# Kernel tuning notes

Hardware: AMD Instinct MI355X
Metric: run time of the kernel (lower is better)

Reference implementation:

```python
import jax, jax.numpy as jnp
import numpy as np

N, D = 8192, 256

def _gram_rbf(x, y, sigma):
    x2 = jnp.sum(x * x, axis=-1)                      # [N]
    y2 = jnp.sum(y * y, axis=-1)                      # [M]
    xy = jnp.einsum('nd,md->nm', x, y)                # [N,M] GEMM
    sq = x2[:, None] + y2[None, :] - 2.0 * xy
    return jnp.exp(-sq / sigma)

def setup_inputs() -> dict:
    key = jax.random.key(0)
    k1, k2 = jax.random.split(key)
    return {
        'input': jax.random.normal(k1, (N, D), dtype=jnp.float32),
        'target': jax.random.normal(k2, (N, D), dtype=jnp.float32) + 0.5,
        'sigma': 256,
    }

def reference(input, target, sigma):
    XX = _gram_rbf(input, input, sigma)
    YY = _gram_rbf(target, target, sigma)
    XY = _gram_rbf(input, target, sigma)
    return jnp.mean(XX) + jnp.mean(YY) - 2.0 * jnp.mean(XY)
```

## Files before the change

### kernel.cpp

```cpp
#include <hip/hip_runtime.h>
#include <hip/hip_bf16.h>
#include <stdint.h>
#include <stddef.h>


#define N_PTS   8192
#define DIM     256
#define TWO_N   16384
#define CSTRIDE 16

#define AS1 __attribute__((address_space(1)))
#define AS3 __attribute__((address_space(3)))

typedef __attribute__((ext_vector_type(4))) float f32x4;

__global__ __launch_bounds__(256) void mmd_prep(const float* __restrict__ X,
                                                const float* __restrict__ Y,
                                                const int* __restrict__ sigmap,
                                                unsigned char* __restrict__ Zf8,
                                                float* __restrict__ n2,
                                                float* __restrict__ out) {
    if (blockIdx.x == 0 && threadIdx.x == 0) out[0] = 0.0f;

    const int wave = threadIdx.x >> 6;
    const int lane = threadIdx.x & 63;
    const int row  = blockIdx.x * 4 + wave;

    const float* src = (row < N_PTS) ? (X + (size_t)row * DIM)
                                     : (Y + (size_t)(row - N_PTS) * DIM);
    float4 v = ((const float4*)src)[lane];

    float s = v.x * v.x + v.y * v.y + v.z * v.z + v.w * v.w;
#pragma unroll
    for (int off = 32; off; off >>= 1) s += __shfl_down(s, off, 64);
    if (lane == 0) {
        const float c2 = -1.4426950408889634f / (float)(*sigmap);
        n2[row] = c2 * s;
    }

    const int p01 = __builtin_amdgcn_cvt_pk_fp8_f32(v.x, v.y, 0, false);
    const int p23 = __builtin_amdgcn_cvt_pk_fp8_f32(v.z, v.w, 0, false);
    const unsigned int pk = ((unsigned)p01 & 0xffffu) | ((unsigned)p23 << 16);
    *(unsigned int*)(Zf8 + (size_t)row * DIM + (size_t)lane * 4) = pk;
}

__global__ __launch_bounds__(256, 2) void mmd_main(const unsigned char* __restrict__ Zf8,
                                                   const float* __restrict__ n2,
                                                   const int* __restrict__ sigmap,
                                                   float* __restrict__ out) {
    __shared__ char smem_b[65536];
    __shared__ float wsum[4];

    const int bid = (int)blockIdx.x;
    const int br  = 127 - (bid >> 4);
    const int cc  = bid & 15;
    if (cc > br) return;

    const int t    = threadIdx.x;
    const int wave = t >> 6;
    const int lane = t & 63;
    const int wm   = wave >> 1;
    const int wn   = wave & 1;
    const int g    = lane >> 4;
    const int ml   = lane & 15;
    const int rowBase = br * 128;

    const float m2 = 2.8853900817779268f / (float)(*sigmap);

    {
        const int colBase0 = cc * 128;
#pragma unroll
        for (int i = 0; i < 8; ++i) {
            const int cidx = i * 256 + t;
            const int col  = cidx >> 4;
            const int s    = cidx & 15;
            const int gc   = s ^ (col & 15);
            const unsigned char* gp = Zf8 + (size_t)(colBase0 + col) * DIM + gc * 16;
            __builtin_amdgcn_global_load_lds((const AS1 void*)gp,
                                             (AS3 void*)(smem_b + (size_t)cidx * 16), 16, 0, 0);
        }
    }

    long af[4][8];
#pragma unroll
    for (int mt = 0; mt < 4; ++mt) {
        const unsigned char* rp =
            Zf8 + (size_t)(rowBase + wm * 64 + mt * 16 + ml) * DIM + g * 8;
#pragma unroll
        for (int kc = 0; kc < 8; ++kc)
            af[mt][kc] = *(const long*)(rp + kc * 32);
    }
    float a_i[4][4];
#pragma unroll
    for (int mt = 0; mt < 4; ++mt)
#pragma unroll
        for (int rr = 0; rr < 4; ++rr)
            a_i[mt][rr] = n2[rowBase + wm * 64 + mt * 16 + g * 4 + rr];

    float block_acc = 0.0f;
    const int brX = (br < 64);
    int cur = 0;

    for (int bc = cc; bc <= br; bc += CSTRIDE) {
        const int colBase = bc * 128;

        float b_j[4];
#pragma unroll
        for (int nt = 0; nt < 4; ++nt)
            b_j[nt] = n2[colBase + wn * 64 + nt * 16 + ml];

        f32x4 acc[4][4] = {};

        __syncthreads();

        if (bc + CSTRIDE <= br) {
            const int colBaseN = colBase + CSTRIDE * 128;
            char* dst = smem_b + (cur ^ 1) * 32768;
#pragma unroll
            for (int i = 0; i < 8; ++i) {
                const int cidx = i * 256 + t;
                const int col  = cidx >> 4;
                const int s    = cidx & 15;
                const int gc   = s ^ (col & 15);
                const unsigned char* gp = Zf8 + (size_t)(colBaseN + col) * DIM + gc * 16;
                __builtin_amdgcn_global_load_lds((const AS1 void*)gp,
                                                 (AS3 void*)(dst + (size_t)cidx * 16), 16, 0, 0);
            }
        }

        const char* buf = smem_b + cur * 32768;
#pragma unroll
        for (int kc = 0; kc < 8; ++kc) {
            const int jp   = kc * 2 + (g >> 1);
            const int half = (g & 1) * 8;
            long bf[4];
#pragma unroll
            for (int nt = 0; nt < 4; ++nt) {
                const int col = wn * 64 + nt * 16 + ml;
                bf[nt] = *(const long*)(buf + (size_t)col * 256
                                            + (size_t)(jp ^ (col & 15)) * 16 + half);
            }
#pragma unroll
            for (int mt = 0; mt < 4; ++mt)
#pragma unroll
                for (int nt = 0; nt < 4; ++nt)
                    acc[mt][nt] = __builtin_amdgcn_mfma_f32_16x16x32_fp8_fp8(
                        af[mt][kc], bf[nt], acc[mt][nt], 0, 0, 0);
        }

        float tsum = 0.0f;
#pragma unroll
        for (int mt = 0; mt < 4; ++mt)
#pragma unroll
            for (int nt = 0; nt < 4; ++nt) {
                const float ab = b_j[nt];
#pragma unroll
                for (int rr = 0; rr < 4; ++rr)
                    tsum += __builtin_amdgcn_exp2f(
                        fmaf(acc[mt][nt][rr], m2, a_i[mt][rr] + ab));
            }

        const float sgn = ((bc < 64) == brX) ? 1.0f : -1.0f;
        const float w   = (bc == br) ? sgn : 2.0f * sgn;
        block_acc = fmaf(w, tsum, block_acc);
        cur ^= 1;
    }

    float s = block_acc;
#pragma unroll
    for (int off = 32; off; off >>= 1) s += __shfl_down(s, off, 64);
    if (lane == 0) wsum[wave] = s;
    __syncthreads();
    if (t == 0)
        atomicAdd(out, (wsum[0] + wsum[1] + wsum[2] + wsum[3]) * (1.0f / 67108864.0f));
}

extern "C" void kernel_launch(void* const* d_in, const int* in_sizes, int n_in,
                              void* d_out, int out_size, void* d_ws, size_t ws_size,
                              hipStream_t stream) {
    const float* X      = (const float*)d_in[0];
    const float* Y      = (const float*)d_in[1];
    const int*   sigmap = (const int*)d_in[2];
    float*       out    = (float*)d_out;

    unsigned char* Zf8 = (unsigned char*)d_ws;
    float*         n2  = (float*)((char*)d_ws + (size_t)TWO_N * DIM);

    mmd_prep<<<TWO_N / 4, 256, 0, stream>>>(X, Y, sigmap, Zf8, n2, out);
    mmd_main<<<128 * CSTRIDE, 256, 0, stream>>>(Zf8, n2, sigmap, out);
}
```

Baseline: 141.5 us.

## Halve LDS by splitting K into two 16KB halves for higher occupancy

Replaces the 64KB double-buffered B tile with a single 32KB buffer holding two K-halves. The second half is loaded while the first is consumed, and the next tile's first half is loaded while the second is consumed. Row norms move from registers to LDS to reduce register pressure, and the launch bound rises from 2 to 3 blocks per SU. The aim is more resident blocks to hide latency, at the cost of an extra barrier per iteration and less prefetch distance.

```diff
diff --git a/kernel.cpp b/kernel.cpp
--- a/kernel.cpp
+++ b/kernel.cpp
@@ -44,11 +44,12 @@
     *(unsigned int*)(Zf8 + (size_t)row * DIM + (size_t)lane * 4) = pk;
 }
 
-__global__ __launch_bounds__(256, 2) void mmd_main(const unsigned char* __restrict__ Zf8,
+__global__ __launch_bounds__(256, 3) void mmd_main(const unsigned char* __restrict__ Zf8,
                                                    const float* __restrict__ n2,
                                                    const int* __restrict__ sigmap,
                                                    float* __restrict__ out) {
-    __shared__ char smem_b[65536];
+    __shared__ char smem_b[32768];
+    __shared__ float n2rS[128];
     __shared__ float wsum[4];
 
     const int bid = (int)blockIdx.x;
@@ -70,16 +71,17 @@
     {
         const int colBase0 = cc * 128;
 #pragma unroll
-        for (int i = 0; i < 8; ++i) {
+        for (int i = 0; i < 4; ++i) {
             const int cidx = i * 256 + t;
-            const int col  = cidx >> 4;
-            const int s    = cidx & 15;
-            const int gc   = s ^ (col & 15);
+            const int col  = cidx >> 3;
+            const int s    = cidx & 7;
+            const int gc   = s ^ (col & 7);
             const unsigned char* gp = Zf8 + (size_t)(colBase0 + col) * DIM + gc * 16;
             __builtin_amdgcn_global_load_lds((const AS1 void*)gp,
                                              (AS3 void*)(smem_b + (size_t)cidx * 16), 16, 0, 0);
         }
     }
+    if (t < 128) n2rS[t] = n2[rowBase + t];
 
     long af[4][8];
 #pragma unroll
@@ -90,16 +92,9 @@
         for (int kc = 0; kc < 8; ++kc)
             af[mt][kc] = *(const long*)(rp + kc * 32);
     }
-    float a_i[4][4];
-#pragma unroll
-    for (int mt = 0; mt < 4; ++mt)
-#pragma unroll
-        for (int rr = 0; rr < 4; ++rr)
-            a_i[mt][rr] = n2[rowBase + wm * 64 + mt * 16 + g * 4 + rr];
 
     float block_acc = 0.0f;
     const int brX = (br < 64);
-    int cur = 0;
 
     for (int bc = cc; bc <= br; bc += CSTRIDE) {
         const int colBase = bc * 128;
@@ -113,57 +108,88 @@
 
         __syncthreads();
 
+#pragma unroll
+        for (int i = 0; i < 4; ++i) {
+            const int cidx = i * 256 + t;
+            const int col  = cidx >> 3;
+            const int s    = cidx & 7;
+            const int gc   = s ^ (col & 7);
+            const unsigned char* gp = Zf8 + (size_t)(colBase + col) * DIM + 128 + gc * 16;
+            __builtin_amdgcn_global_load_lds((const AS1 void*)gp,
+                                             (AS3 void*)(smem_b + 16384 + (size_t)cidx * 16), 16, 0, 0);
+        }
+
+#pragma unroll
+        for (int kc2 = 0; kc2 < 4; ++kc2) {
+            const int jp   = kc2 * 2 + (g >> 1);
+            const int half = (g & 1) * 8;
+            long bf[4];
+#pragma unroll
+            for (int nt = 0; nt < 4; ++nt) {
+                const int col = wn * 64 + nt * 16 + ml;
+                bf[nt] = *(const long*)(smem_b + (size_t)col * 128
+                                            + (size_t)(jp ^ (col & 7)) * 16 + half);
+            }
+#pragma unroll
+            for (int mt = 0; mt < 4; ++mt)
+#pragma unroll
+                for (int nt = 0; nt < 4; ++nt)
+                    acc[mt][nt] = __builtin_amdgcn_mfma_f32_16x16x32_fp8_fp8(
+                        af[mt][kc2], bf[nt], acc[mt][nt], 0, 0, 0);
+        }
+
+        __syncthreads();
+
         if (bc + CSTRIDE <= br) {
             const int colBaseN = colBase + CSTRIDE * 128;
-            char* dst = smem_b + (cur ^ 1) * 32768;
-#pragma unroll
-            for (int i = 0; i < 8; ++i) {
+#pragma unroll
+            for (int i = 0; i < 4; ++i) {
                 const int cidx = i * 256 + t;
-                const int col  = cidx >> 4;
-                const int s    = cidx & 15;
-                const int gc   = s ^ (col & 15);
+                const int col  = cidx >> 3;
+                const int s    = cidx & 7;
+                const int gc   = s ^ (col & 7);
                 const unsigned char* gp = Zf8 + (size_t)(colBaseN + col) * DIM + gc * 16;
                 __builtin_amdgcn_global_load_lds((const AS1 void*)gp,
-                                                 (AS3 void*)(dst + (size_t)cidx * 16), 16, 0, 0);
-            }
-        }
-
-        const char* buf = smem_b + cur * 32768;
-#pragma unroll
-        for (int kc = 0; kc < 8; ++kc) {
-            const int jp   = kc * 2 + (g >> 1);
+                                                 (AS3 void*)(smem_b + (size_t)cidx * 16), 16, 0, 0);
+            }
+        }
+
+#pragma unroll
+        for (int kc2 = 0; kc2 < 4; ++kc2) {
+            const int jp   = kc2 * 2 + (g >> 1);
             const int half = (g & 1) * 8;
             long bf[4];
 #pragma unroll
             for (int nt = 0; nt < 4; ++nt) {
                 const int col = wn * 64 + nt * 16 + ml;
-                bf[nt] = *(const long*)(buf + (size_t)col * 256
-                                            + (size_t)(jp ^ (col & 15)) * 16 + half);
+                bf[nt] = *(const long*)(smem_b + 16384 + (size_t)col * 128
+                                            + (size_t)(jp ^ (col & 7)) * 16 + half);
             }
 #pragma unroll
             for (int mt = 0; mt < 4; ++mt)
 #pragma unroll
                 for (int nt = 0; nt < 4; ++nt)
                     acc[mt][nt] = __builtin_amdgcn_mfma_f32_16x16x32_fp8_fp8(
-                        af[mt][kc], bf[nt], acc[mt][nt], 0, 0, 0);
+                        af[mt][4 + kc2], bf[nt], acc[mt][nt], 0, 0, 0);
         }
 
         float tsum = 0.0f;
 #pragma unroll
-        for (int mt = 0; mt < 4; ++mt)
+        for (int mt = 0; mt < 4; ++mt) {
+            const f32x4 ar = *(const f32x4*)&n2rS[wm * 64 + mt * 16 + g * 4];
 #pragma unroll
             for (int nt = 0; nt < 4; ++nt) {
                 const float ab = b_j[nt];
 #pragma unroll
                 for (int rr = 0; rr < 4; ++rr)
                     tsum += __builtin_amdgcn_exp2f(
-                        fmaf(acc[mt][nt][rr], m2, a_i[mt][rr] + ab));
-            }
+                        fmaf(acc[mt][nt][rr], m2, ar[rr] + ab));
+            }
+        }
 
         const float sgn = ((bc < 64) == brX) ? 1.0f : -1.0f;
         const float w   = (bc == br) ? sgn : 2.0f * sgn;
         block_acc = fmaf(w, tsum, block_acc);
-        cur ^= 1;
     }
 
     float s = block_acc;
```

Result: slower. 172.0 us (+21.6%).
